# Performance work log

Measured on AMD Instinct MI355X. Metric: run time of the kernel, lower is better.

The kernel has to match this reference:

```python
import jax, jax.numpy as jnp
import numpy as np
from jax import lax

DN = ('NHWC', 'HWIO', 'NHWC')

def conv2d(x, w, b):
    return lax.conv_general_dilated(x, w, (1, 1), 'SAME', dimension_numbers=DN) + b

def sdpa(q, k, v):
    # q,k,v: [B, C, L, D]; attend over L with feature dim D
    dk = jnp.asarray(q.shape[-1], dtype=q.dtype)
    scores = jnp.einsum('bcld,bcmd->bclm', q, k) / jnp.sqrt(dk)
    w = jax.nn.softmax(scores, axis=-1)
    return jnp.einsum('bclm,bcmd->bcld', w, v)

def setup_inputs() -> dict:
    key = jax.random.key(0)
    ks = jax.random.split(key, 8)
    B, T, F, N, C = 8, 512, 80, 64, 64
    s = 0.05
    return {
        'q': jax.random.normal(ks[0], (B, T, F, N), jnp.float32),
        'k': jax.random.normal(ks[1], (B, T, F, N), jnp.float32),
        'v': jax.random.normal(ks[2], (B, T, F, N), jnp.float32),
        'wq': jax.random.normal(ks[3], (3, 3, N, C), jnp.float32) * s,
        'bq': jnp.zeros((C,), jnp.float32),
        'wk': jax.random.normal(ks[4], (3, 3, N, C), jnp.float32) * s,
        'bk': jnp.zeros((C,), jnp.float32),
        'wv': jax.random.normal(ks[5], (3, 3, N, C), jnp.float32) * s,
        'bv': jnp.zeros((C,), jnp.float32),
        'wo': jax.random.normal(ks[6], (3, 3, 2 * C, N), jnp.float32) * s,
        'bo': jnp.zeros((N,), jnp.float32),
    }

def reference(q, k, v, wq, bq, wk, bk, wv, bv, wo, bo):
    cq = conv2d(q, wq, bq)  # [B,T,F,C]
    ck = conv2d(k, wk, bk)
    cv = conv2d(v, wv, bv)
    # 'freq' branch: [B,C,T,F], attention over T with feature dim F
    of = sdpa(jnp.transpose(cq, (0, 3, 1, 2)),
              jnp.transpose(ck, (0, 3, 1, 2)),
              jnp.transpose(cv, (0, 3, 1, 2)))  # [B,C,T,F]
    # 'time' branch: [B,C,F,T], attention over F with feature dim T
    ot = sdpa(jnp.transpose(cq, (0, 3, 2, 1)),
              jnp.transpose(ck, (0, 3, 2, 1)),
              jnp.transpose(cv, (0, 3, 2, 1)))  # [B,C,F,T]
    of = jnp.transpose(of, (0, 2, 3, 1))  # [B,T,F,C]
    ot = jnp.transpose(ot, (0, 3, 2, 1))  # [B,T,F,C]
    out = jnp.concatenate([ot, of], axis=-1)  # [B,T,F,2C]
    return conv2d(out, wo, bo)  # [B,T,F,N]
```

## Files before the change

### kernel.cpp

```cpp
#include <hip/hip_runtime.h>
#include <hip/hip_fp16.h>

#define TDIM 512
#define FDIM 80

typedef _Float16 f16x8 __attribute__((ext_vector_type(8)));
typedef _Float16 f16x4 __attribute__((ext_vector_type(4)));
typedef _Float16 f16x2 __attribute__((ext_vector_type(2)));
typedef float f32x4 __attribute__((ext_vector_type(4)));

__global__ __launch_bounds__(256) void k_prep_w(
    const float* __restrict__ wq, const float* __restrict__ wk,
    const float* __restrict__ wv, const float* __restrict__ wo,
    _Float16* __restrict__ wTq, _Float16* __restrict__ wTk,
    _Float16* __restrict__ wTv, _Float16* __restrict__ wTo)
{
  const int total = 3 * 36864 + 73728;
  for (int idx = blockIdx.x * 256 + threadIdx.x; idx < total; idx += gridDim.x * 256) {
    if (idx < 110592) {
      int sel = idx / 36864, r = idx - sel * 36864;
      int ci = r & 63, t2 = r >> 6, co = t2 & 63, kk = t2 >> 6;
      const float* src = (sel == 0) ? wq : (sel == 1) ? wk : wv;
      _Float16* dst = (sel == 0) ? wTq : (sel == 1) ? wTk : wTv;
      dst[r] = (_Float16)src[(kk * 64 + ci) * 64 + co];
    } else {
      int r = idx - 110592;
      int ci = r & 127, t2 = r >> 7, co = t2 & 63, kk = t2 >> 6;
      wTo[r] = (_Float16)wo[(kk * 128 + ci) * 64 + co];
    }
  }
}

__global__ __launch_bounds__(512) void k_conv_in3(
    const float* __restrict__ q, const float* __restrict__ k, const float* __restrict__ v,
    const float* __restrict__ wq, const float* __restrict__ wk, const float* __restrict__ wv,
    const _Float16* __restrict__ wTq, const _Float16* __restrict__ wTk, const _Float16* __restrict__ wTv,
    const float* __restrict__ bq, const float* __restrict__ bk, const float* __restrict__ bv,
    _Float16* __restrict__ yq, _Float16* __restrict__ yk, _Float16* __restrict__ yv)
{
  __shared__ __align__(16) _Float16 xs[328 * 72];
  const int bid = blockIdx.x;
  const int sel = bid >> 11, rest = bid & 2047;
  const float* x = (sel == 0) ? q : (sel == 1) ? k : v;
  const float* w = (sel == 0) ? wq : (sel == 1) ? wk : wv;
  const _Float16* wT = (sel == 0) ? wTq : (sel == 1) ? wTk : wTv;
  const float* bias = (sel == 0) ? bq : (sel == 1) ? bk : bv;
  _Float16* y = (sel == 0) ? yq : (sel == 1) ? yk : yv;

  const int xcd = rest & 7, i = rest >> 3;
  const int b = i >> 5, tp = i & 31;
  const int t0 = (xcd << 6) | (tp << 1);
  const int tid = threadIdx.x;
  const int wvv = tid >> 6, ln = tid & 63;
  const int tsel = wvv >> 2;
  const int lr = ln & 15, lg = ln >> 4;
  const int c0 = (wvv & 3) * 16;

  for (int idx = tid; idx < 328 * 16; idx += 512) {
    int r2 = idx >> 4, cq = idx & 15;
    int rr = r2 / 82, fi = r2 - rr * 82;
    int tt = t0 - 1 + rr, ff = fi - 1;
    f16x4 h;
    #pragma unroll
    for (int j = 0; j < 4; j++) h[j] = (_Float16)0.f;
    if (tt >= 0 && tt < TDIM && ff >= 0 && ff < FDIM) {
      float4 vv = *reinterpret_cast<const float4*>(x + (((b * TDIM + tt) * FDIM + ff) << 6) + cq * 4);
      h[0] = (_Float16)vv.x; h[1] = (_Float16)vv.y; h[2] = (_Float16)vv.z; h[3] = (_Float16)vv.w;
    }
    *reinterpret_cast<f16x4*>(&xs[r2 * 72 + cq * 4]) = h;
  }
  __syncthreads();

  float bvv = bias[c0 + lr];
  f32x4 acc[5];
  #pragma unroll
  for (int mt = 0; mt < 5; mt++)
    #pragma unroll
    for (int r = 0; r < 4; r++) acc[mt][r] = bvv;

  for (int ky = 0; ky < 3; ky++) {
    f16x8 wf[3][2];
    #pragma unroll
    for (int kx = 0; kx < 3; kx++)
      #pragma unroll
      for (int cc = 0; cc < 2; cc++) {
        if (wT) {
          wf[kx][cc] = *reinterpret_cast<const f16x8*>(
              wT + (((ky * 3 + kx) * 64 + c0 + lr) << 6) + cc * 32 + lg * 8);
        } else {
          const float* wp = w + ((ky * 3 + kx) * 64 + cc * 32 + lg * 8) * 64 + c0 + lr;
          #pragma unroll
          for (int j = 0; j < 8; j++) wf[kx][cc][j] = (_Float16)wp[j * 64];
        }
      }
    #pragma unroll
    for (int mt = 0; mt < 5; mt++) {
      #pragma unroll
      for (int kx = 0; kx < 3; kx++) {
        const _Float16* ap = &xs[((tsel + ky) * 82 + mt * 16 + lr + kx) * 72];
        #pragma unroll
        for (int cc = 0; cc < 2; cc++) {
          f16x8 af = *reinterpret_cast<const f16x8*>(ap + cc * 32 + lg * 8);
          acc[mt] = __builtin_amdgcn_mfma_f32_16x16x32_f16(af, wf[kx][cc], acc[mt], 0, 0, 0);
        }
      }
    }
  }

  __syncthreads();
  _Float16* yt = xs + tsel * 5632;
  const int c = c0 + lr;
  #pragma unroll
  for (int mt = 0; mt < 5; mt++) {
    f16x4 h;
    #pragma unroll
    for (int r = 0; r < 4; r++) h[r] = (_Float16)acc[mt][r];
    *reinterpret_cast<f16x4*>(&yt[c * 88 + mt * 16 + lg * 4]) = h;
  }
  __syncthreads();
  #pragma unroll
  for (int kk = 0; kk < 3; kk++) {
    int idx = tid + (kk << 9);
    if (idx < 1280) {
      int ts = idx >= 640, r2 = idx - ts * 640;
      int cc = r2 / 10, f8 = r2 - cc * 10;
      *reinterpret_cast<f16x8*>(y + ((size_t)(b * 64 + cc) * TDIM + t0 + ts) * FDIM + f8 * 8) =
          *reinterpret_cast<const f16x8*>(&xs[ts * 5632 + cc * 88 + f8 * 8]);
    }
  }
}

__global__ __launch_bounds__(512) void k_attn_freq(
    const _Float16* __restrict__ XQ, const _Float16* __restrict__ XK,
    const _Float16* __restrict__ XV, _Float16* __restrict__ CAT)
{
  __shared__ __align__(16) _Float16 Ks[64 * 104];
  __shared__ __align__(16) _Float16 Vt[96 * 72];
  __shared__ __align__(16) _Float16 Pl[8 * 16 * 72];

  const int bid = blockIdx.x;
  const int x8 = bid & 7, kk = bid >> 3;
  const int jj = kk & 7, tl = (kk >> 3) & 3, cc8 = kk >> 5;
  const int bc = x8 + cc8 * 64 + jj * 8;
  const int b = bc >> 6, c = bc & 63;
  const int t0 = tl * 128;
  const int tid = threadIdx.x;
  const int w8 = tid >> 6, ln = tid & 63;
  const int lr = ln & 15, lg = ln >> 4;
  const float qscale = 0.1118033988749895f;
  const float MFIX = 4.0f;

  const _Float16* Qg = XQ + (size_t)bc * 40960 + (size_t)t0 * 80;
  const _Float16* Kg = XK + (size_t)bc * 40960;
  const _Float16* Vg = XV + (size_t)bc * 40960;

  f16x8 qf[3];
  qf[0] = *reinterpret_cast<const f16x8*>(Qg + (w8 * 16 + lr) * 80 + lg * 8);
  qf[1] = *reinterpret_cast<const f16x8*>(Qg + (w8 * 16 + lr) * 80 + 32 + lg * 8);
  {
    f16x8 z;
    #pragma unroll
    for (int j = 0; j < 8; j++) z[j] = (_Float16)0.f;
    qf[2] = (lg < 2) ? *reinterpret_cast<const f16x8*>(Qg + (w8 * 16 + lr) * 80 + 64 + lg * 8) : z;
  }
  #pragma unroll
  for (int kc = 0; kc < 3; kc++)
    #pragma unroll
    for (int j = 0; j < 8; j++) qf[kc][j] = qf[kc][j] * (_Float16)qscale;

  if (tid < 192) {
    int row = tid / 3, cw = tid - row * 3;
    f16x8 z;
    #pragma unroll
    for (int j = 0; j < 8; j++) z[j] = (_Float16)0.f;
    *reinterpret_cast<f16x8*>(&Ks[row * 104 + 80 + cw * 8]) = z;
  }
  if (tid < 144) {
    int rr = tid / 9, cw = tid - rr * 9;
    int row = 80 + rr;
    f16x8 v;
    #pragma unroll
    for (int j = 0; j < 8; j++) v[j] = (row == 80) ? (_Float16)1.f : (_Float16)0.f;
    *reinterpret_cast<f16x8*>(&Vt[row * 72 + cw * 8]) = v;
  }

  const int vm = tid & 63;
  f16x8 kreg0, kreg1;
  f16x2 vreg[5];
  {
    int i0 = tid, r0 = i0 / 10, w0 = i0 - r0 * 10;
    kreg0 = *reinterpret_cast<const f16x8*>(Kg + r0 * 80 + w0 * 8);
    if (tid < 128) {
      int i1 = tid + 512, r1 = i1 / 10, w1 = i1 - r1 * 10;
      kreg1 = *reinterpret_cast<const f16x8*>(Kg + r1 * 80 + w1 * 8);
    }
    #pragma unroll
    for (int s = 0; s < 5; s++)
      vreg[s] = *reinterpret_cast<const f16x2*>(Vg + vm * 80 + (w8 + 8 * s) * 2);
  }

  f32x4 O[6];
  #pragma unroll
  for (int ft = 0; ft < 6; ft++)
    #pragma unroll
    for (int r = 0; r < 4; r++) O[ft][r] = 0.f;

  for (int kt = 0; kt < 8; kt++) {
    __syncthreads();
    {
      int i0 = tid, r0 = i0 / 10, w0 = i0 - r0 * 10;
      *reinterpret_cast<f16x8*>(&Ks[r0 * 104 + w0 * 8]) = kreg0;
      if (tid < 128) {
        int i1 = tid + 512, r1 = i1 / 10, w1 = i1 - r1 * 10;
        *reinterpret_cast<f16x8*>(&Ks[r1 * 104 + w1 * 8]) = kreg1;
      }
      #pragma unroll
      for (int s = 0; s < 5; s++) {
        int f2 = (w8 + 8 * s) * 2;
        Vt[f2 * 72 + vm]       = vreg[s][0];
        Vt[(f2 + 1) * 72 + vm] = vreg[s][1];
      }
    }
    if (kt < 7) {
      const _Float16* Kn = Kg + (kt + 1) * 64 * 80;
      const _Float16* Vn = Vg + (kt + 1) * 64 * 80;
      int i0 = tid, r0 = i0 / 10, w0 = i0 - r0 * 10;
      kreg0 = *reinterpret_cast<const f16x8*>(Kn + r0 * 80 + w0 * 8);
      if (tid < 128) {
        int i1 = tid + 512, r1 = i1 / 10, w1 = i1 - r1 * 10;
        kreg1 = *reinterpret_cast<const f16x8*>(Kn + r1 * 80 + w1 * 8);
      }
      #pragma unroll
      for (int s = 0; s < 5; s++)
        vreg[s] = *reinterpret_cast<const f16x2*>(Vn + vm * 80 + (w8 + 8 * s) * 2);
    }
    __syncthreads();

    f32x4 S[4];
    #pragma unroll
    for (int ms = 0; ms < 4; ms++)
      #pragma unroll
      for (int r = 0; r < 4; r++) S[ms][r] = 0.f;
    __builtin_amdgcn_s_setprio(1);
    #pragma unroll
    for (int kc = 0; kc < 3; kc++) {
      #pragma unroll
      for (int ms = 0; ms < 4; ms++) {
        f16x8 kf = *reinterpret_cast<const f16x8*>(&Ks[(ms * 16 + lr) * 104 + kc * 32 + lg * 8]);
        S[ms] = __builtin_amdgcn_mfma_f32_16x16x32_f16(qf[kc], kf, S[ms], 0, 0, 0);
      }
    }
    __builtin_amdgcn_s_setprio(0);

    _Float16* pw = &Pl[w8 * 16 * 72];
    #pragma unroll
    for (int r = 0; r < 4; r++) {
      int row = lg * 4 + r;
      #pragma unroll
      for (int ms = 0; ms < 4; ms++)
        pw[row * 72 + ((ms * 16 + lr) ^ (lg << 3))] = (_Float16)__expf(S[ms][r] - MFIX);
    }
    asm volatile("s_waitcnt lgkmcnt(0)" ::: "memory");
    const int sx = (lg ^ ((lr >> 2) & 3)) * 8;
    f16x8 pf0 = *reinterpret_cast<const f16x8*>(&pw[lr * 72 + sx]);
    f16x8 pf1 = *reinterpret_cast<const f16x8*>(&pw[lr * 72 + 32 + sx]);

    __builtin_amdgcn_s_setprio(1);
    #pragma unroll
    for (int ft = 0; ft < 6; ft++) {
      f16x8 vf0 = *reinterpret_cast<const f16x8*>(&Vt[(ft * 16 + lr) * 72 + lg * 8]);
      f16x8 vf1 = *reinterpret_cast<const f16x8*>(&Vt[(ft * 16 + lr) * 72 + 32 + lg * 8]);
      O[ft] = __builtin_amdgcn_mfma_f32_16x16x32_f16(pf0, vf0, O[ft], 0, 0, 0);
      O[ft] = __builtin_amdgcn_mfma_f32_16x16x32_f16(pf1, vf1, O[ft], 0, 0, 0);
    }
    __builtin_amdgcn_s_setprio(0);
  }

  float inv[4];
  #pragma unroll
  for (int r = 0; r < 4; r++) {
    float l = __shfl(O[5][r], lg << 4);
    inv[r] = 1.f / l;
  }
  #pragma unroll
  for (int r = 0; r < 4; r++) {
    int t = t0 + w8 * 16 + lg * 4 + r;
    size_t base = ((size_t)(b * 128 + 64 + c) * TDIM + t) * FDIM;
    #pragma unroll
    for (int ft = 0; ft < 5; ft++)
      CAT[base + ft * 16 + lr] = (_Float16)(O[ft][r] * inv[r]);
  }
}

__global__ __launch_bounds__(256) void k_attn_time(
    const _Float16* __restrict__ XQ, const _Float16* __restrict__ XK,
    const _Float16* __restrict__ XV, _Float16* __restrict__ CAT)
{
  __shared__ __align__(16) char smem[70400];
  _Float16* Qt  = (_Float16*)smem;
  _Float16* Kt  = Qt + 80 * 136;
  float*    Sld = (float*)(smem + 43520);
  _Float16* Pld = (_Float16*)smem;

  const int bid = blockIdx.x;
  const int b = bid >> 6, c = bid & 63;
  const int tid = threadIdx.x;
  const int wv = tid >> 6, ln = tid & 63;
  const int lr = ln & 15, lg = ln >> 4;
  const float tscale = 0.04419417382415922f;

  const _Float16* Qg = XQ + (size_t)bid * 40960;
  const _Float16* Kg = XK + (size_t)bid * 40960;
  const _Float16* Vg = XV + (size_t)bid * 40960;

  f32x4 sacc[7];
  #pragma unroll
  for (int i = 0; i < 7; i++)
    #pragma unroll
    for (int r = 0; r < 4; r++) sacc[i][r] = 0.f;

  for (int tc = 0; tc < 4; tc++) {
    __syncthreads();
    for (int idx = tid; idx < 640; idx += 256) {
      int t2 = idx / 10, f8 = idx - t2 * 10;
      int tg = tc * 128 + t2 * 2;
      f16x8 qa = *reinterpret_cast<const f16x8*>(Qg + (size_t)tg * 80 + f8 * 8);
      f16x8 qb = *reinterpret_cast<const f16x8*>(Qg + (size_t)(tg + 1) * 80 + f8 * 8);
      f16x8 ka = *reinterpret_cast<const f16x8*>(Kg + (size_t)tg * 80 + f8 * 8);
      f16x8 kb = *reinterpret_cast<const f16x8*>(Kg + (size_t)(tg + 1) * 80 + f8 * 8);
      #pragma unroll
      for (int j = 0; j < 8; j++) {
        int f = f8 * 8 + j;
        f16x2 qp; qp[0] = qa[j]; qp[1] = qb[j];
        f16x2 kp; kp[0] = ka[j]; kp[1] = kb[j];
        *reinterpret_cast<f16x2*>(&Qt[f * 136 + t2 * 2]) = qp;
        *reinterpret_cast<f16x2*>(&Kt[f * 136 + t2 * 2]) = kp;
      }
    }
    __syncthreads();
    #pragma unroll
    for (int i = 0; i < 7; i++) {
      int ti = wv * 7 + i;
      int te = ti < 25 ? ti : 24;
      int mi = te / 5, ni = te - mi * 5;
      #pragma unroll
      for (int kc = 0; kc < 4; kc++) {
        f16x8 aq = *reinterpret_cast<const f16x8*>(&Qt[(mi * 16 + lr) * 136 + kc * 32 + lg * 8]);
        f16x8 bk = *reinterpret_cast<const f16x8*>(&Kt[(ni * 16 + lr) * 136 + kc * 32 + lg * 8]);
        sacc[i] = __builtin_amdgcn_mfma_f32_16x16x32_f16(aq, bk, sacc[i], 0, 0, 0);
      }
    }
  }
  #pragma unroll
  for (int i = 0; i < 7; i++) {
    int ti = wv * 7 + i;
    if (ti < 25) {
      int mi = ti / 5, ni = ti - mi * 5;
      #pragma unroll
      for (int r = 0; r < 4; r++)
        Sld[(mi * 16 + lg * 4 + r) * 84 + ni * 16 + lr] = sacc[i][r] * tscale;
    }
  }
  __syncthreads();

  {
    const int fy = tid >> 4, gx = tid & 15;
    #pragma unroll
    for (int pass = 0; pass < 5; pass++) {
      int row = pass * 16 + fy;
      float s[5];
      #pragma unroll
      for (int j = 0; j < 5; j++) s[j] = Sld[row * 84 + gx + 16 * j];
      float mx = fmaxf(fmaxf(fmaxf(s[0], s[1]), fmaxf(s[2], s[3])), s[4]);
      #pragma unroll
      for (int sh = 1; sh < 16; sh <<= 1) mx = fmaxf(mx, __shfl_xor(mx, sh, 16));
      float e[5]; float ls = 0.f;
      #pragma unroll
      for (int j = 0; j < 5; j++) { e[j] = __expf(s[j] - mx); ls += e[j]; }
      #pragma unroll
      for (int sh = 1; sh < 16; sh <<= 1) ls += __shfl_xor(ls, sh, 16);
      float inv = 1.f / ls;
      #pragma unroll
      for (int j = 0; j < 5; j++)
        Pld[row * 104 + gx + 16 * j] = (_Float16)(e[j] * inv);
    }
    for (int idx = tid; idx < 240; idx += 256) {
      int row = idx / 3, cw = idx - row * 3;
      f16x8 z;
      #pragma unroll
      for (int j = 0; j < 8; j++) z[j] = (_Float16)0.f;
      *reinterpret_cast<f16x8*>(&Pld[row * 104 + 80 + cw * 8]) = z;
    }
  }
  __syncthreads();

  f16x8 pa[5][3];
  #pragma unroll
  for (int mi = 0; mi < 5; mi++)
    #pragma unroll
    for (int kc = 0; kc < 3; kc++)
      pa[mi][kc] = *reinterpret_cast<const f16x8*>(&Pld[(mi * 16 + lr) * 104 + kc * 32 + lg * 8]);

  _Float16* Ow = (_Float16*)(smem + 43520) + wv * (16 * 88);
  const size_t chbase = (size_t)(b * 128 + c) * TDIM * FDIM;

  #pragma unroll
  for (int j = 0; j < 8; j++) {
    int nt = wv * 8 + j;
    f16x8 vf[3];
    #pragma unroll
    for (int kc = 0; kc < 3; kc++) {
      if (kc < 2) {
        vf[kc] = *reinterpret_cast<const f16x8*>(Vg + (size_t)(nt * 16 + lr) * 80 + kc * 32 + lg * 8);
      } else {
        f16x8 z;
        #pragma unroll
        for (int qq = 0; qq < 8; qq++) z[qq] = (_Float16)0.f;
        vf[kc] = (lg < 2) ? *reinterpret_cast<const f16x8*>(Vg + (size_t)(nt * 16 + lr) * 80 + 64 + lg * 8) : z;
      }
    }
    f32x4 oacc[5];
    #pragma unroll
    for (int mi = 0; mi < 5; mi++)
      #pragma unroll
      for (int r = 0; r < 4; r++) oacc[mi][r] = 0.f;
    #pragma unroll
    for (int mi = 0; mi < 5; mi++)
      #pragma unroll
      for (int kc = 0; kc < 3; kc++)
        oacc[mi] = __builtin_amdgcn_mfma_f32_16x16x32_f16(pa[mi][kc], vf[kc], oacc[mi], 0, 0, 0);

    #pragma unroll
    for (int mi = 0; mi < 5; mi++) {
      f16x4 h;
      #pragma unroll
      for (int r = 0; r < 4; r++) h[r] = (_Float16)oacc[mi][r];
      *reinterpret_cast<f16x4*>(&Ow[lr * 88 + mi * 16 + lg * 4]) = h;
    }
    asm volatile("s_waitcnt lgkmcnt(0)" ::: "memory");
    size_t basec = chbase + (size_t)(nt * 16) * FDIM;
    #pragma unroll
    for (int kk2 = 0; kk2 < 3; kk2++) {
      int idx = ln + (kk2 << 6);
      if (idx < 160) {
        int tl2 = idx / 10, f8 = idx - tl2 * 10;
        *reinterpret_cast<f16x8*>(CAT + basec + tl2 * 80 + f8 * 8) =
            *reinterpret_cast<const f16x8*>(&Ow[tl2 * 88 + f8 * 8]);
      }
    }
  }
}

__global__ __launch_bounds__(512) void k_conv_out(
    const _Float16* __restrict__ x, const float* __restrict__ w,
    const _Float16* __restrict__ wT,
    const float* __restrict__ bias, float* __restrict__ out)
{
  __shared__ __align__(16) _Float16 xs[328 * 72];
  const int bid = blockIdx.x;
  const int xcd = bid & 7, i = bid >> 3;
  const int b = i >> 5, tp = i & 31;
  const int t0 = (xcd << 6) | (tp << 1);
  const int tid = threadIdx.x;
  const int wvv = tid >> 6, ln = tid & 63;
  const int tsel = wvv >> 2;
  const int lr = ln & 15, lg = ln >> 4;
  const int c0 = (wvv & 3) * 16;
  const int t = t0 + tsel;

  float bv = bias[c0 + lr];
  f32x4 acc[5];
  #pragma unroll
  for (int mt = 0; mt < 5; mt++)
    #pragma unroll
    for (int r = 0; r < 4; r++) acc[mt][r] = bv;

  const _Float16* xb = x + (size_t)b * 128 * TDIM * FDIM;

  for (int h = 0; h < 2; h++) {
    __syncthreads();
    {
      int cch = tid & 63, sk = tid >> 6;
      int rr = sk >> 1, side = sk & 1;
      xs[(rr * 82 + side * 81) * 72 + cch] = (_Float16)0.f;
    }
    #pragma unroll
    for (int k = 0; k < 5; k++) {
      int idx = tid + (k << 9);
      int cch = idx & 63, rest = idx >> 6;
      int rr = rest / 10, f8 = rest - rr * 10;
      int tt = t0 - 1 + rr;
      f16x8 hh;
      #pragma unroll
      for (int j = 0; j < 8; j++) hh[j] = (_Float16)0.f;
      if (tt >= 0 && tt < TDIM)
        hh = *reinterpret_cast<const f16x8*>(xb + ((size_t)(h * 64 + cch) * TDIM + tt) * FDIM + f8 * 8);
      #pragma unroll
      for (int j = 0; j < 8; j++)
        xs[(rr * 82 + f8 * 8 + j + 1) * 72 + cch] = hh[j];
    }
    __syncthreads();

    for (int ky = 0; ky < 3; ky++) {
      const int rr = tsel + ky;
      f16x8 wf[3][2];
      #pragma unroll
      for (int kx = 0; kx < 3; kx++)
        #pragma unroll
        for (int cc = 0; cc < 2; cc++) {
          if (wT) {
            wf[kx][cc] = *reinterpret_cast<const f16x8*>(
                wT + (((ky * 3 + kx) * 64 + c0 + lr) << 7) + h * 64 + cc * 32 + lg * 8);
          } else {
            const float* wp = w + ((ky * 3 + kx) * 128 + h * 64 + cc * 32 + lg * 8) * 64 + c0 + lr;
            #pragma unroll
            for (int j = 0; j < 8; j++) wf[kx][cc][j] = (_Float16)wp[j * 64];
          }
        }
      #pragma unroll
      for (int mt = 0; mt < 5; mt++) {
        #pragma unroll
        for (int kx = 0; kx < 3; kx++) {
          const _Float16* ap = &xs[(rr * 82 + mt * 16 + lr + kx) * 72];
          #pragma unroll
          for (int cc = 0; cc < 2; cc++) {
            f16x8 af = *reinterpret_cast<const f16x8*>(ap + cc * 32 + lg * 8);
            acc[mt] = __builtin_amdgcn_mfma_f32_16x16x32_f16(af, wf[kx][cc], acc[mt], 0, 0, 0);
          }
        }
      }
    }
  }

  const int c = c0 + lr;
  #pragma unroll
  for (int mt = 0; mt < 5; mt++) {
    #pragma unroll
    for (int r = 0; r < 4; r++) {
      int f = mt * 16 + lg * 4 + r;
      out[((size_t)(b * TDIM + t) * FDIM + f) * 64 + c] = acc[mt][r];
    }
  }
}

extern "C" void kernel_launch(void* const* d_in, const int* in_sizes, int n_in,
                              void* d_out, int out_size, void* d_ws, size_t ws_size,
                              hipStream_t stream)
{
  const float* q  = (const float*)d_in[0];
  const float* k  = (const float*)d_in[1];
  const float* v  = (const float*)d_in[2];
  const float* wq = (const float*)d_in[3];
  const float* bq = (const float*)d_in[4];
  const float* wk = (const float*)d_in[5];
  const float* bk = (const float*)d_in[6];
  const float* wv = (const float*)d_in[7];
  const float* bv = (const float*)d_in[8];
  const float* wo = (const float*)d_in[9];
  const float* bo = (const float*)d_in[10];

  const size_t PLANE = (size_t)8 * 64 * 512 * 80;
  _Float16* XQh  = (_Float16*)d_ws;
  _Float16* XKh  = XQh + PLANE;
  _Float16* CATh = XKh + PLANE;
  _Float16* XVh  = (_Float16*)d_out;

  _Float16* WT = CATh + 2 * PLANE;
  const size_t need = (4 * PLANE + 184320) * sizeof(_Float16);
  const bool useWT = (ws_size >= need);
  _Float16* wTq = useWT ? WT : nullptr;
  _Float16* wTk = useWT ? WT + 36864 : nullptr;
  _Float16* wTv = useWT ? WT + 73728 : nullptr;
  _Float16* wTo = useWT ? WT + 110592 : nullptr;

  if (useWT)
    hipLaunchKernelGGL(k_prep_w, dim3(180), dim3(256), 0, stream,
                       wq, wk, wv, wo, wTq, wTk, wTv, wTo);

  hipLaunchKernelGGL(k_conv_in3, dim3(6144), dim3(512), 0, stream,
                     q, k, v, wq, wk, wv, wTq, wTk, wTv, bq, bk, bv, XQh, XKh, XVh);
  hipLaunchKernelGGL(k_attn_freq, dim3(2048), dim3(512), 0, stream, XQh, XKh, XVh, CATh);
  hipLaunchKernelGGL(k_attn_time, dim3(512), dim3(256), 0, stream, XQh, XKh, XVh, CATh);
  hipLaunchKernelGGL(k_conv_out, dim3(2048), dim3(512), 0, stream, CATh, wo, wTo, bo, (float*)d_out);
}
```

Baseline: 395.1 us.

## Process four time rows per input-conv block and batch conv_out global loads

The input convolution kernel now computes four output time rows per block instead of two, halving the grid. Each wave handles 32 output channels with two accumulator sets, so every loaded activation fragment feeds two MFMAs. This cuts halo reloads and shared-memory reads per output, at the cost of more registers and fewer blocks. In the output convolution, all five global loads are now issued before any shared-memory stores so their latency overlaps.

Result: slower. 422.3 us (+6.9%).

```diff
diff --git a/kernel.cpp b/kernel.cpp
--- a/kernel.cpp
+++ b/kernel.cpp
@@ -38,9 +38,9 @@
     const float* __restrict__ bq, const float* __restrict__ bk, const float* __restrict__ bv,
     _Float16* __restrict__ yq, _Float16* __restrict__ yk, _Float16* __restrict__ yv)
 {
-  __shared__ __align__(16) _Float16 xs[328 * 72];
+  __shared__ __align__(16) _Float16 xs[6 * 82 * 72];
   const int bid = blockIdx.x;
-  const int sel = bid >> 11, rest = bid & 2047;
+  const int sel = bid >> 10, rest = bid & 1023;
   const float* x = (sel == 0) ? q : (sel == 1) ? k : v;
   const float* w = (sel == 0) ? wq : (sel == 1) ? wk : wv;
   const _Float16* wT = (sel == 0) ? wTq : (sel == 1) ? wTk : wTv;
@@ -48,15 +48,16 @@
   _Float16* y = (sel == 0) ? yq : (sel == 1) ? yk : yv;
 
   const int xcd = rest & 7, i = rest >> 3;
-  const int b = i >> 5, tp = i & 31;
-  const int t0 = (xcd << 6) | (tp << 1);
+  const int b = i >> 4, quad = i & 15;
+  const int t0 = (xcd << 6) | (quad << 2);
   const int tid = threadIdx.x;
   const int wvv = tid >> 6, ln = tid & 63;
-  const int tsel = wvv >> 2;
+  const int tsel = wvv >> 1;
+  const int cH = wvv & 1;
   const int lr = ln & 15, lg = ln >> 4;
-  const int c0 = (wvv & 3) * 16;
-
-  for (int idx = tid; idx < 328 * 16; idx += 512) {
+  const int c0 = cH * 32;
+
+  for (int idx = tid; idx < 7872; idx += 512) {
     int r2 = idx >> 4, cq = idx & 15;
     int rr = r2 / 82, fi = r2 - rr * 82;
     int tt = t0 - 1 + rr, ff = fi - 1;
@@ -71,62 +72,65 @@
   }
   __syncthreads();
 
-  float bvv = bias[c0 + lr];
-  f32x4 acc[5];
+  const float bv0 = bias[c0 + lr];
+  const float bv1 = bias[c0 + 16 + lr];
+  f32x4 acc[5][2];
   #pragma unroll
   for (int mt = 0; mt < 5; mt++)
     #pragma unroll
-    for (int r = 0; r < 4; r++) acc[mt][r] = bvv;
+    for (int r = 0; r < 4; r++) { acc[mt][0][r] = bv0; acc[mt][1][r] = bv1; }
 
   for (int ky = 0; ky < 3; ky++) {
-    f16x8 wf[3][2];
-    #pragma unroll
-    for (int kx = 0; kx < 3; kx++)
+    #pragma unroll
+    for (int kx = 0; kx < 3; kx++) {
       #pragma unroll
       for (int cc = 0; cc < 2; cc++) {
+        f16x8 wf0, wf1;
         if (wT) {
-          wf[kx][cc] = *reinterpret_cast<const f16x8*>(
+          wf0 = *reinterpret_cast<const f16x8*>(
               wT + (((ky * 3 + kx) * 64 + c0 + lr) << 6) + cc * 32 + lg * 8);
+          wf1 = *reinterpret_cast<const f16x8*>(
+              wT + (((ky * 3 + kx) * 64 + c0 + 16 + lr) << 6) + cc * 32 + lg * 8);
         } else {
-          const float* wp = w + ((ky * 3 + kx) * 64 + cc * 32 + lg * 8) * 64 + c0 + lr;
+          const float* wp0 = w + ((ky * 3 + kx) * 64 + cc * 32 + lg * 8) * 64 + c0 + lr;
+          const float* wp1 = wp0 + 16;
           #pragma unroll
-          for (int j = 0; j < 8; j++) wf[kx][cc][j] = (_Float16)wp[j * 64];
+          for (int j = 0; j < 8; j++) { wf0[j] = (_Float16)wp0[j * 64]; wf1[j] = (_Float16)wp1[j * 64]; }
         }
-      }
-    #pragma unroll
-    for (int mt = 0; mt < 5; mt++) {
-      #pragma unroll
-      for (int kx = 0; kx < 3; kx++) {
-        const _Float16* ap = &xs[((tsel + ky) * 82 + mt * 16 + lr + kx) * 72];
         #pragma unroll
-        for (int cc = 0; cc < 2; cc++) {
-          f16x8 af = *reinterpret_cast<const f16x8*>(ap + cc * 32 + lg * 8);
-          acc[mt] = __builtin_amdgcn_mfma_f32_16x16x32_f16(af, wf[kx][cc], acc[mt], 0, 0, 0);
+        for (int mt = 0; mt < 5; mt++) {
+          f16x8 af = *reinterpret_cast<const f16x8*>(
+              &xs[((tsel + ky) * 82 + mt * 16 + lr + kx) * 72 + cc * 32 + lg * 8]);
+          acc[mt][0] = __builtin_amdgcn_mfma_f32_16x16x32_f16(af, wf0, acc[mt][0], 0, 0, 0);
+          acc[mt][1] = __builtin_amdgcn_mfma_f32_16x16x32_f16(af, wf1, acc[mt][1], 0, 0, 0);
         }
       }
     }
   }
 
   __syncthreads();
-  _Float16* yt = xs + tsel * 5632;
-  const int c = c0 + lr;
-  #pragma unroll
-  for (int mt = 0; mt < 5; mt++) {
-    f16x4 h;
-    #pragma unroll
-    for (int r = 0; r < 4; r++) h[r] = (_Float16)acc[mt][r];
-    *reinterpret_cast<f16x4*>(&yt[c * 88 + mt * 16 + lg * 4]) = h;
+  {
+    _Float16* yt = xs + tsel * 5632;
+    #pragma unroll
+    for (int cN = 0; cN < 2; cN++) {
+      int c = c0 + cN * 16 + lr;
+      #pragma unroll
+      for (int mt = 0; mt < 5; mt++) {
+        f16x4 h;
+        #pragma unroll
+        for (int r = 0; r < 4; r++) h[r] = (_Float16)acc[mt][cN][r];
+        *reinterpret_cast<f16x4*>(&yt[c * 88 + mt * 16 + lg * 4]) = h;
+      }
+    }
   }
   __syncthreads();
   #pragma unroll
-  for (int kk = 0; kk < 3; kk++) {
+  for (int kk = 0; kk < 5; kk++) {
     int idx = tid + (kk << 9);
-    if (idx < 1280) {
-      int ts = idx >= 640, r2 = idx - ts * 640;
-      int cc = r2 / 10, f8 = r2 - cc * 10;
-      *reinterpret_cast<f16x8*>(y + ((size_t)(b * 64 + cc) * TDIM + t0 + ts) * FDIM + f8 * 8) =
-          *reinterpret_cast<const f16x8*>(&xs[ts * 5632 + cc * 88 + f8 * 8]);
-    }
+    int ts = idx / 640, r2c = idx - ts * 640;
+    int cc = r2c / 10, f8 = r2c - cc * 10;
+    *reinterpret_cast<f16x8*>(y + ((size_t)(b * 64 + cc) * TDIM + t0 + ts) * FDIM + f8 * 8) =
+        *reinterpret_cast<const f16x8*>(&xs[ts * 5632 + cc * 88 + f8 * 8]);
   }
 }
 
@@ -484,20 +488,26 @@
       int rr = sk >> 1, side = sk & 1;
       xs[(rr * 82 + side * 81) * 72 + cch] = (_Float16)0.f;
     }
-    #pragma unroll
-    for (int k = 0; k < 5; k++) {
-      int idx = tid + (k << 9);
+    f16x8 hb[5];
+    #pragma unroll
+    for (int kk = 0; kk < 5; kk++) {
+      int idx = tid + (kk << 9);
       int cch = idx & 63, rest = idx >> 6;
       int rr = rest / 10, f8 = rest - rr * 10;
       int tt = t0 - 1 + rr;
-      f16x8 hh;
-      #pragma unroll
-      for (int j = 0; j < 8; j++) hh[j] = (_Float16)0.f;
+      #pragma unroll
+      for (int j = 0; j < 8; j++) hb[kk][j] = (_Float16)0.f;
       if (tt >= 0 && tt < TDIM)
-        hh = *reinterpret_cast<const f16x8*>(xb + ((size_t)(h * 64 + cch) * TDIM + tt) * FDIM + f8 * 8);
+        hb[kk] = *reinterpret_cast<const f16x8*>(xb + ((size_t)(h * 64 + cch) * TDIM + tt) * FDIM + f8 * 8);
+    }
+    #pragma unroll
+    for (int kk = 0; kk < 5; kk++) {
+      int idx = tid + (kk << 9);
+      int cch = idx & 63, rest = idx >> 6;
+      int rr = rest / 10, f8 = rest - rr * 10;
       #pragma unroll
       for (int j = 0; j < 8; j++)
-        xs[(rr * 82 + f8 * 8 + j + 1) * 72 + cch] = hh[j];
+        xs[(rr * 82 + f8 * 8 + j + 1) * 72 + cch] = hb[kk][j];
     }
     __syncthreads();
 
@@ -577,7 +587,7 @@
     hipLaunchKernelGGL(k_prep_w, dim3(180), dim3(256), 0, stream,
                        wq, wk, wv, wo, wTq, wTk, wTv, wTo);
 
-  hipLaunchKernelGGL(k_conv_in3, dim3(6144), dim3(512), 0, stream,
+  hipLaunchKernelGGL(k_conv_in3, dim3(3072), dim3(512), 0, stream,
                      q, k, v, wq, wk, wv, wTq, wTk, wTv, bq, bk, bv, XQh, XKh, XVh);
   hipLaunchKernelGGL(k_attn_freq, dim3(2048), dim3(512), 0, stream, XQh, XKh, XVh, CATh);
   hipLaunchKernelGGL(k_attn_time, dim3(512), dim3(256), 0, stream, XQh, XKh, XVh, CATh);
```
